# Performance work log

Hardware: AMD Instinct MI355X
Metric: run time of the kernel (lower is better)

Reference implementation:

```python
import jax, jax.numpy as jnp
import numpy as np

N = 4194304  # number of 3D points (surfels)
H, W = 1024, 1280


def setup_inputs() -> dict:
    key = jax.random.key(0)
    k1, k2, k3 = jax.random.split(key, 3)
    # camera-frame points: x,y in [-0.5, 0.5], z (depth) in [0.5, 2.5]
    xy = jax.random.uniform(k1, (N, 2), dtype=jnp.float32, minval=-0.5, maxval=0.5)
    z = jax.random.uniform(k2, (N, 1), dtype=jnp.float32, minval=0.5, maxval=2.5)
    points = jnp.concatenate([xy, z], axis=-1)
    colors = jax.random.uniform(k3, (N, 3), dtype=jnp.float32)
    fx = fy = 1000.0
    K = jnp.array([[fx, 0.0, W / 2.0], [0.0, fy, H / 2.0], [0.0, 0.0, 1.0]],
                  dtype=jnp.float32)
    return {"points": points, "colors": colors, "K": K, "height": H, "width": W}


def reference(points, colors, K, height, width):
    # pcd2depth: pinhole projection with rounding
    fx, fy, cx, cy = K[0, 0], K[1, 1], K[0, 2], K[1, 2]
    z = points[:, 2]
    u = jnp.round(fx * points[:, 0] / z + cx).astype(jnp.int32)
    v = jnp.round(fy * points[:, 1] / z + cy).astype(jnp.int32)
    valid = (z > 0) & (u >= 0) & (u < width) & (v >= 0) & (v < height)
    n = points.shape[0]
    npix = height * width
    # sentinel pixel npix for invalid points
    flat = jnp.where(valid, v * width + u, npix)
    # far-to-near overwrite after depth_sort=True)
    order = jnp.argsort(jnp.where(valid, z, jnp.inf))  # ascending depth
    flat_sorted = flat[order]
    ranks = jnp.arange(n, dtype=jnp.int32)
    # per-pixel min rank (rank = position in depth-ascending order)
    win = jnp.full(npix + 1, n, dtype=jnp.int32).at[flat_sorted].min(ranks)
    win = win[:npix]
    has_point = win < n
    winner = order[jnp.minimum(win, n - 1)]  # point index per pixel
    img = jnp.where(has_point[:, None], colors[winner].astype(jnp.float32), 0.0)
    return img.reshape(height, width, 3)
```

## Files before the change

### kernel.cpp

```cpp
#include <hip/hip_runtime.h>
#include <stdint.h>

#define NPTS    4194304
#define IMG_H   1024
#define IMG_W   1280
#define NPIX    (IMG_H * IMG_W)

#define TW      80
#define TH      32
#define TILES_X (IMG_W / TW)
#define TILES_Y (IMG_H / TH)
#define NBINS   (TILES_X * TILES_Y)
#define TPIX    (TW * TH)

#define NBLK    768
#define TPB     256
#define SEGS_PER_THREAD (NBLK / TPB)

#define CHUNK_Q ((NPTS / 4 + NBLK - 1) / NBLK)
#define CHUNK_P (CHUNK_Q * 4)
#define SSTRIDE CHUNK_P

static const unsigned long long KEY_SENTINEL = ~0ULL;
#define KEY47_MASK ((1ULL << 47) - 1)


struct Perm { unsigned short p[NBINS]; };
constexpr Perm make_perm() {
    Perm P{};
    float score[NBINS] = {};
    for (int i = 0; i < NBINS; ++i) {
        int tx = i % TILES_X, ty = i / TILES_X;
        float du = ((float)tx + 0.5f) * (float)TW - 640.0f;
        float dv = ((float)ty + 0.5f) * (float)TH - 512.0f;
        du /= 640.0f; dv /= 512.0f;
        score[i] = du * du + dv * dv;
        P.p[i] = (unsigned short)i;
    }
    for (int i = 1; i < NBINS; ++i) {
        unsigned short key = P.p[i];
        float ks = score[key];
        int j = i - 1;
        while (j >= 0 && score[P.p[j]] > ks) { P.p[j + 1] = P.p[j]; --j; }
        P.p[j + 1] = key;
    }
    return P;
}
__device__ __constant__ Perm c_perm = make_perm();

__device__ __forceinline__ bool project(float x, float y, float z,
                                        float fx, float fy, float cx, float cy,
                                        int& u, int& v) {
    float uf = rintf(fx * x / z + cx);
    float vf = rintf(fy * y / z + cy);
    bool valid = (z > 0.0f) &&
                 (uf >= 0.0f) && (uf < (float)IMG_W) &&
                 (vf >= 0.0f) && (vf < (float)IMG_H);
    u = (int)uf;
    v = (int)vf;
    return valid;
}

__device__ __forceinline__ unsigned int zc_of(float z) {
    unsigned int zb = __float_as_uint(z);
    unsigned int zc = zb - 0x3F000000u;
    if ((int)zc < 0) zc = 0;
    if (zc > 0x1FFFFFFu) zc = 0x1FFFFFFu;
    return zc;
}

__global__ __launch_bounds__(TPB) void pass_bin(
        const float4* __restrict__ pts4, const float* __restrict__ Kmat,
        unsigned int* __restrict__ cnt_off ,
        unsigned long long* __restrict__ grec ,
        int n_quads, int qchunk) {
    __shared__ unsigned long long srec[CHUNK_P];
    __shared__ unsigned int hist[NBINS];
    __shared__ unsigned int cur[NBINS];
    __shared__ unsigned int tsum[TPB];

    int t   = threadIdx.x;
    int blk = blockIdx.x;
#pragma unroll
    for (int i = t; i < NBINS; i += TPB) hist[i] = 0;
    __syncthreads();

    float fx = Kmat[0], cx = Kmat[2];
    float fy = Kmat[4], cy = Kmat[5];

    int q0 = blk * qchunk;
    int q1 = min(n_quads, q0 + qchunk);

    for (int q = q0 + t; q < q1; q += TPB) {
        float4 a = pts4[3 * q + 0];
        float4 b = pts4[3 * q + 1];
        float4 c = pts4[3 * q + 2];
        float px[4] = {a.x, a.w, b.z, c.y};
        float py[4] = {a.y, b.x, b.w, c.z};
        float pz[4] = {a.z, b.y, c.x, c.w};
#pragma unroll
        for (int k = 0; k < 4; ++k) {
            int u, v;
            if (project(px[k], py[k], pz[k], fx, fy, cx, cy, u, v)) {
                int bin = (v >> 5) * TILES_X + (u / TW);
                atomicAdd(&hist[bin], 1u);
            }
        }
    }
    __syncthreads();

    unsigned int hv[2];
    {
#pragma unroll
        for (int j = 0; j < 2; ++j) hv[j] = hist[2 * t + j];
        tsum[t] = hv[0] + hv[1];
    }
    __syncthreads();
    for (int off = 1; off < TPB; off <<= 1) {
        unsigned int x = (t >= off) ? tsum[t - off] : 0u;
        __syncthreads();
        tsum[t] += x;
        __syncthreads();
    }
    {
        unsigned int run = (t > 0) ? tsum[t - 1] : 0u;
#pragma unroll
        for (int j = 0; j < 2; ++j) {
            cur[2 * t + j] = run;
            run += hv[j];
        }
    }
    __syncthreads();

#pragma unroll
    for (int i = t; i < NBINS; i += TPB)
        cnt_off[(size_t)blk * NBINS + i] = (hist[i] << 16) | cur[i];
    __syncthreads();

    for (int q = q0 + t; q < q1; q += TPB) {
        float4 a = pts4[3 * q + 0];
        float4 b = pts4[3 * q + 1];
        float4 c = pts4[3 * q + 2];
        float px[4] = {a.x, a.w, b.z, c.y};
        float py[4] = {a.y, b.x, b.w, c.z};
        float pz[4] = {a.z, b.y, c.x, c.w};
        unsigned int i0 = 4u * (unsigned int)q;
#pragma unroll
        for (int k = 0; k < 4; ++k) {
            int u, v;
            if (project(px[k], py[k], pz[k], fx, fy, cx, cy, u, v)) {
                int tx  = u / TW;
                int bin = (v >> 5) * TILES_X + tx;
                unsigned int pos = (unsigned int)((v & 31) * TW + (u - tx * TW));
                unsigned int slot = atomicAdd(&cur[bin], 1u);
                srec[slot] = ((unsigned long long)pos << 47) |
                             ((unsigned long long)zc_of(pz[k]) << 22) |
                             (i0 + (unsigned int)k);
            }
        }
    }
    __syncthreads();

    unsigned int nrec = cur[NBINS - 1];
    unsigned long long* my = grec + (size_t)blk * SSTRIDE;
    for (unsigned int i = t; i < nrec; i += TPB) my[i] = srec[i];
}

__global__ __launch_bounds__(TPB) void pass_render(
        const unsigned long long* __restrict__ grec,
        const unsigned int* __restrict__ cnt_off,
        const float* __restrict__ colors,
        float* __restrict__ out) {
    __shared__ unsigned long long key[TPIX];

    int t = threadIdx.x;
    int b = c_perm.p[blockIdx.x];

#pragma unroll
    for (int i = t; i < TPIX; i += TPB) key[i] = KEY_SENTINEL;
    __syncthreads();

#pragma unroll
    for (int s = 0; s < SEGS_PER_THREAD; ++s) {
        int blk = t + s * TPB;
        unsigned int w   = cnt_off[(size_t)blk * NBINS + b];
        unsigned int cnt = w >> 16;
        unsigned int off = w & 0xFFFFu;
        const unsigned long long* seg = grec + (size_t)blk * SSTRIDE + off;
        unsigned int r = 0;
        for (; r + 4 <= cnt; r += 4) {
            unsigned long long r0 = seg[r + 0];
            unsigned long long r1 = seg[r + 1];
            unsigned long long r2 = seg[r + 2];
            unsigned long long r3 = seg[r + 3];
            atomicMin(&key[(unsigned int)(r0 >> 47)], r0 & KEY47_MASK);
            atomicMin(&key[(unsigned int)(r1 >> 47)], r1 & KEY47_MASK);
            atomicMin(&key[(unsigned int)(r2 >> 47)], r2 & KEY47_MASK);
            atomicMin(&key[(unsigned int)(r3 >> 47)], r3 & KEY47_MASK);
        }
        for (; r < cnt; ++r) {
            unsigned long long rec = seg[r];
            atomicMin(&key[(unsigned int)(rec >> 47)], rec & KEY47_MASK);
        }
    }
    __syncthreads();

    int tx = b % TILES_X, ty = b / TILES_X;
#pragma unroll
    for (int i = t; i < TPIX; i += TPB) {
        int row = i / TW, col = i - row * TW;
        unsigned long long kk = key[i];
        float r = 0.0f, g = 0.0f, bl = 0.0f;
        if (kk != KEY_SENTINEL) {
            unsigned int idx = (unsigned int)(kk & 0x3FFFFFu);
            r  = colors[3 * idx + 0];
            g  = colors[3 * idx + 1];
            bl = colors[3 * idx + 2];
        }
        size_t gp = (size_t)(ty * TH + row) * IMG_W + (size_t)(tx * TW + col);
        out[3 * gp + 0] = r;
        out[3 * gp + 1] = g;
        out[3 * gp + 2] = bl;
    }
}

__global__ void init_keys_vec(ulonglong2* __restrict__ keys, int n_vec2) {
    int i = blockIdx.x * blockDim.x + threadIdx.x;
    if (i < n_vec2) keys[i] = ulonglong2{~0ULL, ~0ULL};
}

__global__ void scatter_points_pretest(const float4* __restrict__ pts4,
                                       const float* __restrict__ Kmat,
                                       unsigned long long* __restrict__ keys,
                                       int n_quads) {
    int t = blockIdx.x * blockDim.x + threadIdx.x;
    if (t >= n_quads) return;
    float fx = Kmat[0], cx = Kmat[2];
    float fy = Kmat[4], cy = Kmat[5];
    float4 a = pts4[3 * t + 0];
    float4 b = pts4[3 * t + 1];
    float4 c = pts4[3 * t + 2];
    float px[4] = {a.x, a.w, b.z, c.y};
    float py[4] = {a.y, b.x, b.w, c.z};
    float pz[4] = {a.z, b.y, c.x, c.w};
    unsigned int i0 = 4u * (unsigned int)t;
#pragma unroll
    for (int k = 0; k < 4; ++k) {
        int u, v;
        if (!project(px[k], py[k], pz[k], fx, fy, cx, cy, u, v)) continue;
        int pix = v * IMG_W + u;
        unsigned long long key =
            ((unsigned long long)__float_as_uint(pz[k]) << 32) | (i0 + k);
        if (key < keys[pix]) atomicMin(&keys[pix], key);
    }
}

__global__ void resolve_pixels4(const unsigned long long* __restrict__ keys,
                                const float* __restrict__ colors,
                                float* __restrict__ out, int n_quads) {
    int t = blockIdx.x * blockDim.x + threadIdx.x;
    if (t >= n_quads) return;
    int base = 4 * t;
    ulonglong2 k01 = *(const ulonglong2*)(keys + base);
    ulonglong2 k23 = *(const ulonglong2*)(keys + base + 2);
    unsigned long long kk[4] = {k01.x, k01.y, k23.x, k23.y};
    float c[12];
#pragma unroll
    for (int j = 0; j < 4; ++j) {
        float r = 0.0f, g = 0.0f, b = 0.0f;
        if (kk[j] != KEY_SENTINEL) {
            unsigned int idx = (unsigned int)(kk[j] & 0xFFFFFFFFu);
            r = colors[3 * idx + 0];
            g = colors[3 * idx + 1];
            b = colors[3 * idx + 2];
        }
        c[3 * j + 0] = r; c[3 * j + 1] = g; c[3 * j + 2] = b;
    }
    float4* o = (float4*)(out + 3 * (size_t)base);
    o[0] = float4{c[0], c[1], c[2],  c[3]};
    o[1] = float4{c[4], c[5], c[6],  c[7]};
    o[2] = float4{c[8], c[9], c[10], c[11]};
}

extern "C" void kernel_launch(void* const* d_in, const int* in_sizes, int n_in,
                              void* d_out, int out_size, void* d_ws, size_t ws_size,
                              hipStream_t stream) {
    const float4* pts4  = (const float4*)d_in[0];
    const float* colors = (const float*)d_in[1];
    const float* Kmat   = (const float*)d_in[2];
    float* out = (float*)d_out;

    int n       = in_sizes[0] / 3;
    int n_quads = n / 4;
    int qchunk  = (n_quads + NBLK - 1) / NBLK;

    char* ws = (char*)d_ws;
    unsigned int*       cnt_off = (unsigned int*)ws;
    size_t tbl_bytes = (size_t)NBLK * NBINS * sizeof(unsigned int);
    unsigned long long* grec =
        (unsigned long long*)(ws + ((tbl_bytes + 63) & ~(size_t)63));
    size_t need = ((tbl_bytes + 63) & ~(size_t)63) +
                  (size_t)NBLK * SSTRIDE * sizeof(unsigned long long);

    if (qchunk <= CHUNK_Q && ws_size >= need) {
        pass_bin<<<NBLK, TPB, 0, stream>>>(pts4, Kmat, cnt_off, grec,
                                           n_quads, qchunk);
        pass_render<<<NBINS, TPB, 0, stream>>>(grec, cnt_off, colors, out);
    } else {
        unsigned long long* keys = (unsigned long long*)d_ws;
        const int B = 256;
        int n_vec2 = NPIX / 2;
        init_keys_vec<<<(n_vec2 + B - 1) / B, B, 0, stream>>>(
            (ulonglong2*)keys, n_vec2);
        scatter_points_pretest<<<(n_quads + B - 1) / B, B, 0, stream>>>(
            pts4, Kmat, keys, n_quads);
        int npix_quads = NPIX / 4;
        resolve_pixels4<<<(npix_quads + B - 1) / B, B, 0, stream>>>(
            keys, colors, out, npix_quads);
    }
}
```

Baseline: 172.6 us.

## Cache projections in LDS, scatter via index permutation, transpose count table

The binning kernel now stages each point's projected bin, pixel and depth in shared memory during the histogram pass. The scatter pass then reads from there instead of reloading and reprojecting the points, and builds a 16-bit index permutation. The final write packs the records through that permutation into coalesced global stores. A new transpose kernel turns the per-block count/offset table bin-major, so the render kernel reads it contiguously. The cost is more shared memory per block, which may lower occupancy, plus an extra kernel launch.

```diff
diff --git a/kernel.cpp b/kernel.cpp
--- a/kernel.cpp
+++ b/kernel.cpp
@@ -23,6 +23,7 @@
 
 static const unsigned long long KEY_SENTINEL = ~0ULL;
 #define KEY47_MASK ((1ULL << 47) - 1)
+#define STAGE_INVALID (1ULL << 63)
 
 
 struct Perm { unsigned short p[NBINS]; };
@@ -75,9 +76,11 @@
         unsigned long long* __restrict__ grec ,
         int n_quads, int qchunk) {
     __shared__ unsigned long long srec[CHUNK_P];
+    __shared__ unsigned short iperm[CHUNK_P];
     __shared__ unsigned int hist[NBINS];
     __shared__ unsigned int cur[NBINS];
     __shared__ unsigned int tsum[TPB];
+    __shared__ unsigned int s_total;
 
     int t   = threadIdx.x;
     int blk = blockIdx.x;
@@ -98,13 +101,20 @@
         float px[4] = {a.x, a.w, b.z, c.y};
         float py[4] = {a.y, b.x, b.w, c.z};
         float pz[4] = {a.z, b.y, c.x, c.w};
+        int ql = q - q0;
 #pragma unroll
         for (int k = 0; k < 4; ++k) {
             int u, v;
+            unsigned long long w = STAGE_INVALID;
             if (project(px[k], py[k], pz[k], fx, fy, cx, cy, u, v)) {
-                int bin = (v >> 5) * TILES_X + (u / TW);
+                int tx  = u / TW;
+                int bin = (v >> 5) * TILES_X + tx;
+                unsigned int pos = (unsigned int)((v & 31) * TW + (u - tx * TW));
+                w = ((unsigned long long)bin << 37) |
+                    ((unsigned long long)pos << 25) | zc_of(pz[k]);
                 atomicAdd(&hist[bin], 1u);
             }
+            srec[k * CHUNK_Q + ql] = w;
         }
     }
     __syncthreads();
@@ -129,6 +139,7 @@
             cur[2 * t + j] = run;
             run += hv[j];
         }
+        if (t == TPB - 1) s_total = run;
     }
     __syncthreads();
 
@@ -138,37 +149,51 @@
     __syncthreads();
 
     for (int q = q0 + t; q < q1; q += TPB) {
-        float4 a = pts4[3 * q + 0];
-        float4 b = pts4[3 * q + 1];
-        float4 c = pts4[3 * q + 2];
-        float px[4] = {a.x, a.w, b.z, c.y};
-        float py[4] = {a.y, b.x, b.w, c.z};
-        float pz[4] = {a.z, b.y, c.x, c.w};
-        unsigned int i0 = 4u * (unsigned int)q;
+        int ql = q - q0;
 #pragma unroll
         for (int k = 0; k < 4; ++k) {
-            int u, v;
-            if (project(px[k], py[k], pz[k], fx, fy, cx, cy, u, v)) {
-                int tx  = u / TW;
-                int bin = (v >> 5) * TILES_X + tx;
-                unsigned int pos = (unsigned int)((v & 31) * TW + (u - tx * TW));
-                unsigned int slot = atomicAdd(&cur[bin], 1u);
-                srec[slot] = ((unsigned long long)pos << 47) |
-                             ((unsigned long long)zc_of(pz[k]) << 22) |
-                             (i0 + (unsigned int)k);
+            int js = k * CHUNK_Q + ql;
+            unsigned long long w = srec[js];
+            if (!(w >> 63)) {
+                int bin = (int)(w >> 37);
+                unsigned int s = atomicAdd(&cur[bin], 1u);
+                iperm[s] = (unsigned short)js;
             }
         }
     }
     __syncthreads();
 
-    unsigned int nrec = cur[NBINS - 1];
+    unsigned int nrec = s_total;
     unsigned long long* my = grec + (size_t)blk * SSTRIDE;
-    for (unsigned int i = t; i < nrec; i += TPB) my[i] = srec[i];
+    for (unsigned int g = t; g < nrec; g += TPB) {
+        int js = iperm[g];
+        unsigned long long w = srec[js];
+        unsigned int pos = (unsigned int)((w >> 25) & 0xFFFu);
+        unsigned int zc  = (unsigned int)(w & 0x1FFFFFFu);
+        int ql = js % CHUNK_Q;
+        int k  = js / CHUNK_Q;
+        unsigned int idx = 4u * (unsigned int)(q0 + ql) + (unsigned int)k;
+        my[g] = ((unsigned long long)pos << 47) |
+                ((unsigned long long)zc << 22) | idx;
+    }
+}
+
+__global__ __launch_bounds__(1024) void transpose_tbl(
+        const unsigned int* __restrict__ in,
+        unsigned int* __restrict__ outT) {
+    __shared__ unsigned int tile[32][33];
+    int x = blockIdx.x * 32 + threadIdx.x;
+    int y = blockIdx.y * 32 + threadIdx.y;
+    tile[threadIdx.y][threadIdx.x] = in[(size_t)y * NBINS + x];
+    __syncthreads();
+    int ox = blockIdx.y * 32 + threadIdx.x;
+    int oy = blockIdx.x * 32 + threadIdx.y;
+    outT[(size_t)oy * NBLK + ox] = tile[threadIdx.x][threadIdx.y];
 }
 
 __global__ __launch_bounds__(TPB) void pass_render(
         const unsigned long long* __restrict__ grec,
-        const unsigned int* __restrict__ cnt_off,
+        const unsigned int* __restrict__ cnt_offT ,
         const float* __restrict__ colors,
         float* __restrict__ out) {
     __shared__ unsigned long long key[TPIX];
@@ -183,7 +208,7 @@
 #pragma unroll
     for (int s = 0; s < SEGS_PER_THREAD; ++s) {
         int blk = t + s * TPB;
-        unsigned int w   = cnt_off[(size_t)blk * NBINS + b];
+        unsigned int w   = cnt_offT[(size_t)b * NBLK + blk];
         unsigned int cnt = w >> 16;
         unsigned int off = w & 0xFFFFu;
         const unsigned long long* seg = grec + (size_t)blk * SSTRIDE + off;
@@ -295,17 +320,23 @@
     int qchunk  = (n_quads + NBLK - 1) / NBLK;
 
     char* ws = (char*)d_ws;
-    unsigned int*       cnt_off = (unsigned int*)ws;
-    size_t tbl_bytes = (size_t)NBLK * NBINS * sizeof(unsigned int);
+    size_t off = 0;
+    auto alloc = [&](size_t bytes) {
+        char* p = ws + off;
+        off += (bytes + 63) & ~(size_t)63;
+        return p;
+    };
+    unsigned int*       cnt_off  = (unsigned int*)alloc((size_t)NBLK * NBINS * 4);
+    unsigned int*       cnt_offT = (unsigned int*)alloc((size_t)NBINS * NBLK * 4);
     unsigned long long* grec =
-        (unsigned long long*)(ws + ((tbl_bytes + 63) & ~(size_t)63));
-    size_t need = ((tbl_bytes + 63) & ~(size_t)63) +
-                  (size_t)NBLK * SSTRIDE * sizeof(unsigned long long);
-
-    if (qchunk <= CHUNK_Q && ws_size >= need) {
+        (unsigned long long*)alloc((size_t)NBLK * SSTRIDE * 8);
+
+    if (qchunk <= CHUNK_Q && ws_size >= off) {
         pass_bin<<<NBLK, TPB, 0, stream>>>(pts4, Kmat, cnt_off, grec,
                                            n_quads, qchunk);
-        pass_render<<<NBINS, TPB, 0, stream>>>(grec, cnt_off, colors, out);
+        transpose_tbl<<<dim3(NBINS / 32, NBLK / 32), dim3(32, 32), 0, stream>>>(
+            cnt_off, cnt_offT);
+        pass_render<<<NBINS, TPB, 0, stream>>>(grec, cnt_offT, colors, out);
     } else {
         unsigned long long* keys = (unsigned long long*)d_ws;
         const int B = 256;
```

New measurement: 178.7 us. +3.5%, slower.
